# Kernel tuning notes

Measured on AMD Instinct MI355X. Metric: run time of the kernel, lower is better.

Reference implementation:

```python
import jax, jax.numpy as jnp
import numpy as np

EPS = 1e-5
KH = KW = 3
PAD = 1

def conv3x3(x, w, b=None):
    out = jax.lax.conv_general_dilated(
        x, w, window_strides=(1, 1), padding=((PAD, PAD), (PAD, PAD)),
        dimension_numbers=("NCHW", "OIHW", "NCHW"))
    if b is not None:
        out = out + b[None, :, None, None]
    return out

def batchnorm(x, gamma, beta):
    # training-mode BatchNorm2d: batch statistics over (N, H, W)
    mean = x.mean(axis=(0, 2, 3), keepdims=True)
    var = x.var(axis=(0, 2, 3), keepdims=True)
    return gamma[None, :, None, None] * (x - mean) / jnp.sqrt(var + EPS) + beta[None, :, None, None]

def bilinear_gather(x, y_pos, x_pos):
    # x: [B,C,H,W]; y_pos/x_pos: [B,P,H,W] (P = KH*KW sampling taps)
    # zero padding outside image (mmcv modulated deform conv semantics)
    B, C, H, W = x.shape
    P = y_pos.shape[1]
    x_flat = x.reshape(B, C, H * W)
    y0 = jnp.floor(y_pos)
    x0 = jnp.floor(x_pos)
    ly = y_pos - y0
    lx = x_pos - x0
    out = jnp.zeros((B, C, P, H, W), dtype=x.dtype)
    for dy, dx, wgt in ((0, 0, (1 - ly) * (1 - lx)), (0, 1, (1 - ly) * lx),
                        (1, 0, ly * (1 - lx)), (1, 1, ly * lx)):
        yi = y0 + dy
        xi = x0 + dx
        valid = ((yi >= 0) & (yi <= H - 1) & (xi >= 0) & (xi <= W - 1)).astype(x.dtype)
        yc = jnp.clip(yi, 0, H - 1).astype(jnp.int32)
        xc = jnp.clip(xi, 0, W - 1).astype(jnp.int32)
        idx = (yc * W + xc).reshape(B, 1, P * H * W)
        vals = jnp.take_along_axis(x_flat, jnp.broadcast_to(idx, (B, C, P * H * W)), axis=2)
        vals = vals.reshape(B, C, P, H, W)
        out = out + vals * (wgt * valid)[:, None]
    return out  # [B,C,P,H,W]

def modulated_deform_conv(x, w_off, b_off, w_dcn):
    B, C, H, W = x.shape
    P = KH * KW
    off = conv3x3(x, w_off, b_off)  # [B, 3*P, H, W]
    o1, o2, m = jnp.split(off, 3, axis=1)
    offset = jnp.concatenate([o1, o2], axis=1)            # [B, 2P, H, W]
    offset = offset.reshape(B, P, 2, H, W)                # channel 2p -> dy, 2p+1 -> dx
    mask = jax.nn.sigmoid(m)                              # [B, P, H, W]
    hh = jnp.arange(H, dtype=x.dtype)
    ww = jnp.arange(W, dtype=x.dtype)
    ky = jnp.arange(KH, dtype=x.dtype)
    kx = jnp.arange(KW, dtype=x.dtype)
    # base sampling grid per tap p = ky*KW + kx: (h - PAD + ky, w - PAD + kx)
    base_y = (hh[None, :] - PAD + ky[:, None])            # [KH, H]
    base_x = (ww[None, :] - PAD + kx[:, None])            # [KW, W]
    base_y = jnp.broadcast_to(base_y[:, None, :, None], (KH, KW, H, W)).reshape(P, H, W)
    base_x = jnp.broadcast_to(base_x[None, :, None, :], (KH, KW, H, W)).reshape(P, H, W)
    y_pos = base_y[None] + offset[:, :, 0]                # [B,P,H,W]
    x_pos = base_x[None] + offset[:, :, 1]
    sampled = bilinear_gather(x, y_pos, x_pos)            # [B,C,P,H,W]
    sampled = sampled * mask[:, None]
    w = w_dcn.reshape(w_dcn.shape[0], C, P)               # [O, C, P]
    return jnp.einsum("bcphw,ocp->bohw", sampled, w)

def setup_inputs() -> dict:
    key = jax.random.key(0)
    ks = jax.random.split(key, 10)
    B, Ch, H, W = 4, 256, 64, 64
    Cin, Cout = 2 * Ch, 256
    P = KH * KW
    inp = {
        "input_v": jax.random.normal(ks[0], (B, Ch, H, W), jnp.float32),
        "input_i": jax.random.normal(ks[1], (B, Ch, H, W), jnp.float32),
        "w_off": jax.random.normal(ks[2], (3 * P, Cin, KH, KW), jnp.float32) * 0.01,
        "b_off": jnp.zeros((3 * P,), jnp.float32),
        "w_dcn": jax.random.normal(ks[3], (Cout, Cin, KH, KW), jnp.float32) * (1.0 / np.sqrt(Cin * P)),
        "gamma1": jnp.ones((Cout,), jnp.float32),
        "beta1": jnp.zeros((Cout,), jnp.float32),
        "w2": jax.random.normal(ks[4], (Cout, Cout, KH, KW), jnp.float32) * (1.0 / np.sqrt(Cout * P)),
        "gamma2": jnp.ones((Cout,), jnp.float32),
        "beta2": jnp.zeros((Cout,), jnp.float32),
    }
    return inp

def reference(input_v, input_i, w_off, b_off, w_dcn, gamma1, beta1, w2, gamma2, beta2):
    x = jnp.concatenate([input_v, input_i], axis=1)
    out = modulated_deform_conv(x, w_off, b_off, w_dcn)
    out = jax.nn.relu(batchnorm(out, gamma1, beta1))
    out = jax.nn.relu(batchnorm(conv3x3(out, w2), gamma2, beta2))
    return out
```

## Files before the change

### kernel.cpp

```cpp
#include <hip/hip_runtime.h>
#include <cstdint>
#include <cstddef>

typedef unsigned short u16;
typedef __attribute__((ext_vector_type(8))) short s16x8;
typedef __attribute__((ext_vector_type(4))) float f32x4;

#define DEV __device__ __forceinline__

DEV float bf2f(short u){
  union { unsigned int i; float f; } v;
  v.i = ((unsigned int)(u16)u) << 16;
  return v.f;
}
DEV short f2bf(float f){
  union { float f; unsigned int i; } v; v.f = f;
  unsigned int u = v.i;
  u += 0x7fffu + ((u >> 16) & 1u);
  return (short)(u >> 16);
}
DEV s16x8 s16x8_zero(){
  s16x8 z;
#pragma unroll
  for(int j=0;j<8;j++) z[j]=0;
  return z;
}
DEV f32x4 f32x4_zero(){
  f32x4 z;
#pragma unroll
  for(int j=0;j<4;j++) z[j]=0.f;
  return z;
}
DEV f32x4 mfma16(s16x8 a, s16x8 b, f32x4 c){
  return __builtin_amdgcn_mfma_f32_16x16x32_bf16(a, b, c, 0, 0, 0);
}

static constexpr size_t OFF_ACC_B  = 0;
static constexpr size_t OUT1_ACC_B = 2097152;
static constexpr size_t OUT2_ACC_B = OUT1_ACC_B + 16777216;
static constexpr size_t STATS_B    = OUT2_ACC_B + 16777216;
static constexpr size_t ZERO_BYTES = STATS_B + 4096;
static constexpr size_t XN_B       = ZERO_BYTES;
static constexpr size_t OUT1N_B    = XN_B + 16777216;
static constexpr size_t WOFFT_B    = OUT1N_B + 8388608;
static constexpr size_t WDCNT_B    = WOFFT_B + 294912;
static constexpr size_t W2T_B      = WDCNT_B + 2359296;

__global__ void k_x_to_nhwc(const float* __restrict__ v, const float* __restrict__ vi,
                            u16* __restrict__ xn){
  __shared__ float tile[64][65];
  const int b = blockIdx.z, c0 = blockIdx.y*64, hw0 = blockIdx.x*64;
  const float* src = (c0 < 256) ? (v  + ((size_t)b*256 + c0)      *4096)
                                : (vi + ((size_t)b*256 + (c0-256))*4096);
  const int t = threadIdx.x;
#pragma unroll
  for(int k=0;k<16;k++){
    int idx = t + k*256;
    int cl = idx >> 6, wl = idx & 63;
    tile[cl][wl] = src[(size_t)cl*4096 + hw0 + wl];
  }
  __syncthreads();
#pragma unroll
  for(int k=0;k<16;k++){
    int idx = t + k*256;
    int wl = idx >> 6, cl = idx & 63;
    xn[(size_t)(b*4096 + hw0 + wl)*512 + c0 + cl] = (u16)f2bf(tile[cl][wl]);
  }
}

__global__ void k_prep_woff(const float* __restrict__ w, u16* __restrict__ wt){
  int idx = blockIdx.x*256 + threadIdx.x;
  if(idx >= 32*4608) return;
  int n = idx / 4608, k = idx % 4608;
  int t = k >> 9, c = k & 511;
  float val = (n < 27) ? w[(size_t)(n*512 + c)*9 + t] : 0.f;
  wt[idx] = (u16)f2bf(val);
}
__global__ void k_prep_wdcn(const float* __restrict__ w, u16* __restrict__ wt){
  int idx = blockIdx.x*256 + threadIdx.x;
  if(idx >= 256*4608) return;
  int n = idx / 4608, k = idx % 4608;
  int t = k >> 9, c = k & 511;
  wt[idx] = (u16)f2bf(w[(size_t)(n*512 + c)*9 + t]);
}
__global__ void k_prep_w2(const float* __restrict__ w, u16* __restrict__ wt){
  int idx = blockIdx.x*256 + threadIdx.x;
  if(idx >= 256*2304) return;
  int n = idx / 2304, k = idx % 2304;
  int t = k >> 8, c = k & 255;
  wt[idx] = (u16)f2bf(w[(size_t)(n*256 + c)*9 + t]);
}

__global__ __launch_bounds__(256, 2) void k_conv_off(
    const u16* __restrict__ xn, const u16* __restrict__ wt, float* __restrict__ offa){
  __shared__ short A_lds[4][128][8];
  __shared__ short B_lds[4][32][8];
  const int tid = threadIdx.x;
  const int lane = tid & 63, wid = tid >> 6;
  const int quad = lane >> 4, ln = lane & 15;
  const int m0 = blockIdx.x * 128;
  const int b = m0 >> 12;
  const int h0 = (m0 & 4095) >> 6;
  const int ks = blockIdx.y;
  const int ts0 = (ks==0)?0:(ks==1)?2:(ks==2)?4:6;
  const int ts1 = (ks==0)?2:(ks==1)?4:(ks==2)?6:9;
  const int m_base = wid * 32;
  const int r = tid >> 1, sp = (tid & 1) * 2;
  const int h_r = h0 + (r >> 6), w_r = r & 63;
  const s16x8* Ap = (const s16x8*)A_lds;
  const s16x8* Bp = (const s16x8*)B_lds;
  f32x4 acc[2][2];
#pragma unroll
  for(int mf=0;mf<2;mf++)
#pragma unroll
    for(int nf=0;nf<2;nf++) acc[mf][nf] = f32x4_zero();

  for(int tp=ts0; tp<ts1; tp++){
    const int ty = tp/3, tx = tp - ty*3;
    const int y = h_r - 1 + ty, x = w_r - 1 + tx;
    const bool vld = (y>=0) & (y<64) & (x>=0) & (x<64);
    const u16* src = xn + (long)(b*4096 + y*64 + x)*512 + sp*8;
    const int kbase = tp*512;
    for(int cc=0; cc<16; cc++){
      const int c0 = cc*32;
      s16x8 v0 = s16x8_zero(), v1 = s16x8_zero();
      if(vld){
        v0 = *(const s16x8*)(src + c0);
        v1 = *(const s16x8*)(src + c0 + 8);
      }
      *(s16x8*)(&A_lds[sp][r][0])   = v0;
      *(s16x8*)(&A_lds[sp+1][r][0]) = v1;
      if(tid < 128){
        const int n = tid & 31, s2 = tid >> 5;
        *(s16x8*)(&B_lds[s2][n][0]) =
            *(const s16x8*)(wt + (size_t)n*4608 + kbase + c0 + s2*8);
      }
      __syncthreads();
      s16x8 a0 = Ap[quad*128 + m_base + ln];
      s16x8 a1 = Ap[quad*128 + m_base + 16 + ln];
      s16x8 b0 = Bp[quad*32 + ln];
      s16x8 b1 = Bp[quad*32 + 16 + ln];
      acc[0][0] = mfma16(a0, b0, acc[0][0]);
      acc[0][1] = mfma16(a0, b1, acc[0][1]);
      acc[1][0] = mfma16(a1, b0, acc[1][0]);
      acc[1][1] = mfma16(a1, b1, acc[1][1]);
      __syncthreads();
    }
  }
#pragma unroll
  for(int mf=0;mf<2;mf++)
#pragma unroll
    for(int nf=0;nf<2;nf++){
      const int col = nf*16 + ln;
#pragma unroll
      for(int i=0;i<4;i++){
        const int row = m_base + mf*16 + quad*4 + i;
        unsafeAtomicAdd(offa + (size_t)(m0+row)*32 + col, acc[mf][nf][i]);
      }
    }
}

__global__ __launch_bounds__(256, 2) void k_dcn(
    const u16* __restrict__ xn, const u16* __restrict__ wt,
    const float* __restrict__ offa, const float* __restrict__ boff,
    float* __restrict__ outa){
  __shared__ short A_lds[4][64][8];
  __shared__ short B_lds[4][256][8];
  __shared__ int   p_ofs[4][64];
  __shared__ float p_wgt[4][64];
  const int tid = threadIdx.x;
  const int lane = tid & 63, wid = tid >> 6;
  const int quad = lane >> 4, ln = lane & 15;
  const int m0 = blockIdx.x * 64;
  const int b = m0 >> 12;
  const int h = (m0 & 4095) >> 6;
  const int ts0 = blockIdx.y ? 4 : 0;
  const int ts1 = blockIdx.y ? 9 : 4;
  const int wm = wid >> 1, wn = wid & 1;
  const int m_base = wm*32, n_base = wn*128;
  const int r = tid >> 2, sub = tid & 3;
  const s16x8* Ap = (const s16x8*)A_lds;
  const s16x8* Bp = (const s16x8*)B_lds;
  f32x4 acc[2][8];
#pragma unroll
  for(int mf=0;mf<2;mf++)
#pragma unroll
    for(int nf=0;nf<8;nf++) acc[mf][nf] = f32x4_zero();

  for(int tp=ts0; tp<ts1; tp++){
    if(tid < 64){
      const int rr = tid;
      const float* orow = offa + (size_t)(m0+rr)*32;
      float dy = orow[2*tp]   + boff[2*tp];
      float dx = orow[2*tp+1] + boff[2*tp+1];
      float mz = orow[18+tp]  + boff[18+tp];
      float mk = 1.f / (1.f + expf(-mz));
      float ypos = (float)(h - 1 + tp/3) + dy;
      float xpos = (float)(rr - 1 + tp%3) + dx;
      float y0f = floorf(ypos), x0f = floorf(xpos);
      float ly = ypos - y0f, lx = xpos - x0f;
      int y0 = (int)y0f, x0 = (int)x0f;
#pragma unroll
      for(int k=0;k<4;k++){
        int ddy = k >> 1, ddx = k & 1;
        int yi = y0 + ddy, xi = x0 + ddx;
        bool vv = (yi >= 0) & (yi < 64) & (xi >= 0) & (xi < 64);
        float wk = (ddy ? ly : 1.f-ly) * (ddx ? lx : 1.f-lx) * mk;
        if(!vv) wk = 0.f;
        int yc = yi < 0 ? 0 : (yi > 63 ? 63 : yi);
        int xc = xi < 0 ? 0 : (xi > 63 ? 63 : xi);
        p_ofs[k][rr] = ((b << 12) + (yc << 6) + xc) << 9;
        p_wgt[k][rr] = wk;
      }
    }
    __syncthreads();
    const float w0f = p_wgt[0][r], w1f = p_wgt[1][r], w2f = p_wgt[2][r], w3f = p_wgt[3][r];
    const u16* s0p = xn + p_ofs[0][r] + sub*8;
    const u16* s1p = xn + p_ofs[1][r] + sub*8;
    const u16* s2p = xn + p_ofs[2][r] + sub*8;
    const u16* s3p = xn + p_ofs[3][r] + sub*8;
    const u16* wrow0 = wt + (size_t)tid*4608 + tp*512;

    for(int cc=0; cc<16; cc++){
      const int c0 = cc*32;
      s16x8 v0 = *(const s16x8*)(s0p + c0);
      s16x8 v1 = *(const s16x8*)(s1p + c0);
      s16x8 v2 = *(const s16x8*)(s2p + c0);
      s16x8 v3 = *(const s16x8*)(s3p + c0);
      s16x8 pk;
#pragma unroll
      for(int j=0;j<8;j++){
        float f = w0f * bf2f(v0[j]);
        f = fmaf(w1f, bf2f(v1[j]), f);
        f = fmaf(w2f, bf2f(v2[j]), f);
        f = fmaf(w3f, bf2f(v3[j]), f);
        pk[j] = f2bf(f);
      }
      *(s16x8*)(&A_lds[sub][r][0]) = pk;
#pragma unroll
      for(int s2=0; s2<4; s2++)
        *(s16x8*)(&B_lds[s2][tid][0]) = *(const s16x8*)(wrow0 + c0 + s2*8);
      __syncthreads();
      s16x8 af0 = Ap[quad*64 + m_base + ln];
      s16x8 af1 = Ap[quad*64 + m_base + 16 + ln];
      s16x8 bfr[8];
#pragma unroll
      for(int nf=0;nf<8;nf++) bfr[nf] = Bp[quad*256 + n_base + nf*16 + ln];
#pragma unroll
      for(int nf=0;nf<8;nf++){
        acc[0][nf] = mfma16(af0, bfr[nf], acc[0][nf]);
        acc[1][nf] = mfma16(af1, bfr[nf], acc[1][nf]);
      }
      __syncthreads();
    }
  }
#pragma unroll
  for(int mf=0;mf<2;mf++)
#pragma unroll
    for(int nf=0;nf<8;nf++){
      const int col = n_base + nf*16 + ln;
#pragma unroll
      for(int i=0;i<4;i++){
        const int row = m_base + mf*16 + quad*4 + i;
        unsafeAtomicAdd(outa + (size_t)(m0+row)*256 + col, acc[mf][nf][i]);
      }
    }
}

__global__ __launch_bounds__(256, 2) void k_conv2(
    const u16* __restrict__ a_in, const u16* __restrict__ wt, float* __restrict__ outa){
  __shared__ short A_lds[4][64][8];
  __shared__ short B_lds[4][256][8];
  const int tid = threadIdx.x;
  const int lane = tid & 63, wid = tid >> 6;
  const int quad = lane >> 4, ln = lane & 15;
  const int m0 = blockIdx.x * 64;
  const int b = m0 >> 12;
  const int h = (m0 & 4095) >> 6;
  const int ts0 = blockIdx.y ? 4 : 0;
  const int ts1 = blockIdx.y ? 9 : 4;
  const int wm = wid >> 1, wn = wid & 1;
  const int m_base = wm*32, n_base = wn*128;
  const int r = tid >> 2, sub = tid & 3;
  const s16x8* Ap = (const s16x8*)A_lds;
  const s16x8* Bp = (const s16x8*)B_lds;
  f32x4 acc[2][8];
#pragma unroll
  for(int mf=0;mf<2;mf++)
#pragma unroll
    for(int nf=0;nf<8;nf++) acc[mf][nf] = f32x4_zero();

  for(int tp=ts0; tp<ts1; tp++){
    const int ty = tp/3, tx = tp - ty*3;
    const int y = h - 1 + ty, x = r - 1 + tx;
    const bool vld = (y>=0) & (y<64) & (x>=0) & (x<64);
    const u16* src = a_in + (long)(b*4096 + y*64 + x)*256 + sub*8;
    const u16* wrow0 = wt + (size_t)tid*2304 + tp*256;
    for(int cc=0; cc<8; cc++){
      const int c0 = cc*32;
      s16x8 va = vld ? *(const s16x8*)(src + c0) : s16x8_zero();
      *(s16x8*)(&A_lds[sub][r][0]) = va;
#pragma unroll
      for(int s2=0;s2<4;s2++)
        *(s16x8*)(&B_lds[s2][tid][0]) = *(const s16x8*)(wrow0 + c0 + s2*8);
      __syncthreads();
      s16x8 af0 = Ap[quad*64 + m_base + ln];
      s16x8 af1 = Ap[quad*64 + m_base + 16 + ln];
      s16x8 bfr[8];
#pragma unroll
      for(int nf=0;nf<8;nf++) bfr[nf] = Bp[quad*256 + n_base + nf*16 + ln];
#pragma unroll
      for(int nf=0;nf<8;nf++){
        acc[0][nf] = mfma16(af0, bfr[nf], acc[0][nf]);
        acc[1][nf] = mfma16(af1, bfr[nf], acc[1][nf]);
      }
      __syncthreads();
    }
  }
#pragma unroll
  for(int mf=0;mf<2;mf++)
#pragma unroll
    for(int nf=0;nf<8;nf++){
      const int col = n_base + nf*16 + ln;
#pragma unroll
      for(int i=0;i<4;i++){
        const int row = m_base + mf*16 + quad*4 + i;
        unsafeAtomicAdd(outa + (size_t)(m0+row)*256 + col, acc[mf][nf][i]);
      }
    }
}

__global__ void k_stats(const float* __restrict__ acc, float* __restrict__ sum,
                        float* __restrict__ sq){
  const int m0 = blockIdx.x*64;
  const int c = threadIdx.x;
  float s = 0.f, q = 0.f;
  for(int i=0;i<64;i++){
    float v = acc[(size_t)(m0+i)*256 + c];
    s += v; q += v*v;
  }
  unsafeAtomicAdd(sum + c, s);
  unsafeAtomicAdd(sq + c, q);
}

__global__ void k_bn1(const float* __restrict__ acc, const float* __restrict__ sum,
                      const float* __restrict__ sq, const float* __restrict__ g,
                      const float* __restrict__ bt, u16* __restrict__ o){
  __shared__ float sc[256], sh[256];
  const int t = threadIdx.x;
  {
    float mean = sum[t] * (1.f/16384.f);
    float var  = sq[t] * (1.f/16384.f) - mean*mean;
    float rstd = rsqrtf(var + 1e-5f);
    float s = g[t] * rstd;
    sc[t] = s; sh[t] = bt[t] - mean*s;
  }
  __syncthreads();
  const int c4 = (t & 63) * 4;
  const float s0 = sc[c4], s1 = sc[c4+1], s2 = sc[c4+2], s3 = sc[c4+3];
  const float h0 = sh[c4], h1 = sh[c4+1], h2 = sh[c4+2], h3 = sh[c4+3];
#pragma unroll
  for(int k=0;k<4;k++){
    int m = blockIdx.x*16 + k*4 + (t>>6);
    const float4 v = *(const float4*)(acc + (size_t)m*256 + c4);
    unsigned int lo = (unsigned int)(u16)f2bf(fmaxf(0.f, v.x*s0 + h0))
                    | ((unsigned int)(u16)f2bf(fmaxf(0.f, v.y*s1 + h1)) << 16);
    unsigned int hi = (unsigned int)(u16)f2bf(fmaxf(0.f, v.z*s2 + h2))
                    | ((unsigned int)(u16)f2bf(fmaxf(0.f, v.w*s3 + h3)) << 16);
    uint2 pr; pr.x = lo; pr.y = hi;
    *(uint2*)(o + (size_t)m*256 + c4) = pr;
  }
}

__global__ void k_bn2_out(const float* __restrict__ acc, const float* __restrict__ sum,
                          const float* __restrict__ sq, const float* __restrict__ g,
                          const float* __restrict__ bt, float* __restrict__ out){
  __shared__ float tile[64][65];
  __shared__ float sc[64], sh[64];
  const int t = threadIdx.x;
  const int b = blockIdx.z, c0 = blockIdx.y*64, hw0 = blockIdx.x*64;
  if(t < 64){
    int c = c0 + t;
    float mean = sum[c] * (1.f/16384.f);
    float var  = sq[c] * (1.f/16384.f) - mean*mean;
    float rstd = rsqrtf(var + 1e-5f);
    float s = g[c] * rstd;
    sc[t] = s; sh[t] = bt[c] - mean*s;
  }
  __syncthreads();
#pragma unroll
  for(int k=0;k<16;k++){
    int idx = t + k*256;
    int wl = idx >> 6, cl = idx & 63;
    float v = acc[(size_t)((b<<12) + hw0 + wl)*256 + c0 + cl];
    tile[wl][cl] = fmaxf(0.f, v*sc[cl] + sh[cl]);
  }
  __syncthreads();
#pragma unroll
  for(int k=0;k<16;k++){
    int idx = t + k*256;
    int cl = idx >> 6, wl = idx & 63;
    out[(size_t)(b*256 + c0 + cl)*4096 + hw0 + wl] = tile[wl][cl];
  }
}

extern "C" void kernel_launch(void* const* d_in, const int* in_sizes, int n_in,
                              void* d_out, int out_size, void* d_ws, size_t ws_size,
                              hipStream_t stream){
  const float* in_v  = (const float*)d_in[0];
  const float* in_i  = (const float*)d_in[1];
  const float* w_off = (const float*)d_in[2];
  const float* b_off = (const float*)d_in[3];
  const float* w_dcn = (const float*)d_in[4];
  const float* g1    = (const float*)d_in[5];
  const float* bt1   = (const float*)d_in[6];
  const float* w2    = (const float*)d_in[7];
  const float* g2    = (const float*)d_in[8];
  const float* bt2   = (const float*)d_in[9];
  float* out = (float*)d_out;
  char* ws = (char*)d_ws;

  float* off_acc  = (float*)(ws + OFF_ACC_B);
  float* out1_acc = (float*)(ws + OUT1_ACC_B);
  float* out2_acc = (float*)(ws + OUT2_ACC_B);
  float* stats    = (float*)(ws + STATS_B);
  float* sum1 = stats,       *sq1 = stats + 256;
  float* sum2 = stats + 512, *sq2 = stats + 768;
  u16* xn    = (u16*)(ws + XN_B);
  u16* out1n = (u16*)(ws + OUT1N_B);
  u16* wofft = (u16*)(ws + WOFFT_B);
  u16* wdcnt = (u16*)(ws + WDCNT_B);
  u16* w2t   = (u16*)(ws + W2T_B);

  hipMemsetAsync(ws, 0, ZERO_BYTES, stream);
  k_x_to_nhwc<<<dim3(64,8,4), 256, 0, stream>>>(in_v, in_i, xn);
  k_prep_woff<<<576, 256, 0, stream>>>(w_off, wofft);
  k_prep_wdcn<<<4608, 256, 0, stream>>>(w_dcn, wdcnt);
  k_prep_w2<<<2304, 256, 0, stream>>>(w2, w2t);
  k_conv_off<<<dim3(128,4), 256, 0, stream>>>(xn, wofft, off_acc);
  k_dcn<<<dim3(256,2), 256, 0, stream>>>(xn, wdcnt, off_acc, b_off, out1_acc);
  k_stats<<<256, 256, 0, stream>>>(out1_acc, sum1, sq1);
  k_bn1<<<1024, 256, 0, stream>>>(out1_acc, sum1, sq1, g1, bt1, out1n);
  k_conv2<<<dim3(256,2), 256, 0, stream>>>(out1n, w2t, out2_acc);
  k_stats<<<256, 256, 0, stream>>>(out2_acc, sum2, sq2);
  k_bn2_out<<<dim3(64,4,4), 256, 0, stream>>>(out2_acc, sum2, sq2, g2, bt2, out);
}
```

Measured before the change: 377.3 us.

## Software-pipeline global loads and split channels across more blocks in conv kernels

Restructures the three GEMM-style conv kernels (offset conv, deformable conv, conv2) so the next iteration's global loads are issued into registers before the LDS stores and MFMA work of the current one, hiding memory latency behind compute. Each grid doubles by splitting the input-channel range in half, and the results are combined through the existing atomic accumulation. Launch bounds go from 2 to 4 blocks per SU to raise occupancy, and the deformable kernel now computes bilinear offsets and weights for all taps up front instead of per tap. The costs are more atomic traffic, extra registers for prefetched values, and redundant per-block offset computation.

```diff
diff --git a/kernel.cpp b/kernel.cpp
--- a/kernel.cpp
+++ b/kernel.cpp
@@ -91,7 +91,7 @@
   wt[idx] = (u16)f2bf(w[(size_t)(n*256 + c)*9 + t]);
 }
 
-__global__ __launch_bounds__(256, 2) void k_conv_off(
+__global__ __launch_bounds__(256, 4) void k_conv_off(
     const u16* __restrict__ xn, const u16* __restrict__ wt, float* __restrict__ offa){
   __shared__ short A_lds[4][128][8];
   __shared__ short B_lds[4][32][8];
@@ -101,9 +101,11 @@
   const int m0 = blockIdx.x * 128;
   const int b = m0 >> 12;
   const int h0 = (m0 & 4095) >> 6;
-  const int ks = blockIdx.y;
-  const int ts0 = (ks==0)?0:(ks==1)?2:(ks==2)?4:6;
-  const int ts1 = (ks==0)?2:(ks==1)?4:(ks==2)?6:9;
+  const int ks = blockIdx.y >> 1;
+  const int chh = blockIdx.y & 1;
+  const int CH0 = chh << 8;
+  const int ts0 = (ks == 3) ? 6 : ks*2;
+  const int ntap = (ks == 3) ? 3 : 2;
   const int m_base = wid * 32;
   const int r = tid >> 1, sp = (tid & 1) * 2;
   const int h_r = h0 + (r >> 6), w_r = r & 63;
@@ -115,37 +117,45 @@
 #pragma unroll
     for(int nf=0;nf<2;nf++) acc[mf][nf] = f32x4_zero();
 
-  for(int tp=ts0; tp<ts1; tp++){
+  s16x8 v0, v1, bv;
+  auto load_it = [&](int it){
+    const int tp = ts0 + (it >> 3);
     const int ty = tp/3, tx = tp - ty*3;
     const int y = h_r - 1 + ty, x = w_r - 1 + tx;
     const bool vld = (y>=0) & (y<64) & (x>=0) & (x<64);
-    const u16* src = xn + (long)(b*4096 + y*64 + x)*512 + sp*8;
-    const int kbase = tp*512;
-    for(int cc=0; cc<16; cc++){
-      const int c0 = cc*32;
-      s16x8 v0 = s16x8_zero(), v1 = s16x8_zero();
-      if(vld){
-        v0 = *(const s16x8*)(src + c0);
-        v1 = *(const s16x8*)(src + c0 + 8);
-      }
-      *(s16x8*)(&A_lds[sp][r][0])   = v0;
-      *(s16x8*)(&A_lds[sp+1][r][0]) = v1;
-      if(tid < 128){
-        const int n = tid & 31, s2 = tid >> 5;
-        *(s16x8*)(&B_lds[s2][n][0]) =
-            *(const s16x8*)(wt + (size_t)n*4608 + kbase + c0 + s2*8);
-      }
-      __syncthreads();
-      s16x8 a0 = Ap[quad*128 + m_base + ln];
-      s16x8 a1 = Ap[quad*128 + m_base + 16 + ln];
-      s16x8 b0 = Bp[quad*32 + ln];
-      s16x8 b1 = Bp[quad*32 + 16 + ln];
-      acc[0][0] = mfma16(a0, b0, acc[0][0]);
-      acc[0][1] = mfma16(a0, b1, acc[0][1]);
-      acc[1][0] = mfma16(a1, b0, acc[1][0]);
-      acc[1][1] = mfma16(a1, b1, acc[1][1]);
-      __syncthreads();
-    }
+    const int cA = CH0 + (it & 7)*32;
+    v0 = s16x8_zero(); v1 = s16x8_zero();
+    if(vld){
+      const u16* src = xn + ((size_t)((b<<12) + (y<<6) + x) << 9) + cA + sp*8;
+      v0 = *(const s16x8*)(src);
+      v1 = *(const s16x8*)(src + 8);
+    }
+    if(tid < 128){
+      const int n = tid & 31, s2 = tid >> 5;
+      bv = *(const s16x8*)(wt + (size_t)n*4608 + tp*512 + cA + s2*8);
+    }
+  };
+
+  const int NIT = ntap * 8;
+  load_it(0);
+  for(int it = 0; it < NIT; ++it){
+    __syncthreads();
+    *(s16x8*)(&A_lds[sp][r][0])   = v0;
+    *(s16x8*)(&A_lds[sp+1][r][0]) = v1;
+    if(tid < 128){
+      const int n = tid & 31, s2 = tid >> 5;
+      *(s16x8*)(&B_lds[s2][n][0]) = bv;
+    }
+    if(it + 1 < NIT) load_it(it + 1);
+    __syncthreads();
+    s16x8 a0 = Ap[quad*128 + m_base + ln];
+    s16x8 a1 = Ap[quad*128 + m_base + 16 + ln];
+    s16x8 b0 = Bp[quad*32 + ln];
+    s16x8 b1 = Bp[quad*32 + 16 + ln];
+    acc[0][0] = mfma16(a0, b0, acc[0][0]);
+    acc[0][1] = mfma16(a0, b1, acc[0][1]);
+    acc[1][0] = mfma16(a1, b0, acc[1][0]);
+    acc[1][1] = mfma16(a1, b1, acc[1][1]);
   }
 #pragma unroll
   for(int mf=0;mf<2;mf++)
@@ -160,37 +170,42 @@
     }
 }
 
-__global__ __launch_bounds__(256, 2) void k_dcn(
+__global__ __launch_bounds__(256, 4) void k_dcn(
     const u16* __restrict__ xn, const u16* __restrict__ wt,
     const float* __restrict__ offa, const float* __restrict__ boff,
     float* __restrict__ outa){
   __shared__ short A_lds[4][64][8];
   __shared__ short B_lds[4][256][8];
-  __shared__ int   p_ofs[4][64];
-  __shared__ float p_wgt[4][64];
+  __shared__ int   p_ofs[5][4][64];
+  __shared__ float p_wgt[5][4][64];
   const int tid = threadIdx.x;
   const int lane = tid & 63, wid = tid >> 6;
   const int quad = lane >> 4, ln = lane & 15;
   const int m0 = blockIdx.x * 64;
   const int b = m0 >> 12;
   const int h = (m0 & 4095) >> 6;
-  const int ts0 = blockIdx.y ? 4 : 0;
-  const int ts1 = blockIdx.y ? 9 : 4;
+  const int tg = blockIdx.y >> 1;
+  const int chh = blockIdx.y & 1;
+  const int CH0 = chh << 8;
+  const int ts0 = tg ? 4 : 0;
+  const int ntap = tg ? 5 : 4;
   const int wm = wid >> 1, wn = wid & 1;
   const int m_base = wm*32, n_base = wn*128;
   const int r = tid >> 2, sub = tid & 3;
   const s16x8* Ap = (const s16x8*)A_lds;
   const s16x8* Bp = (const s16x8*)B_lds;
+  const u16* wrowt = wt + (size_t)tid*4608;
   f32x4 acc[2][8];
 #pragma unroll
   for(int mf=0;mf<2;mf++)
 #pragma unroll
     for(int nf=0;nf<8;nf++) acc[mf][nf] = f32x4_zero();
 
-  for(int tp=ts0; tp<ts1; tp++){
-    if(tid < 64){
-      const int rr = tid;
-      const float* orow = offa + (size_t)(m0+rr)*32;
+  {
+    const int rr = tid & 63;
+    const float* orow = offa + (size_t)(m0+rr)*32;
+    for(int tpi = tid >> 6; tpi < ntap; tpi += 4){
+      const int tp = ts0 + tpi;
       float dy = orow[2*tp]   + boff[2*tp];
       float dx = orow[2*tp+1] + boff[2*tp+1];
       float mz = orow[18+tp]  + boff[18+tp];
@@ -209,49 +224,64 @@
         if(!vv) wk = 0.f;
         int yc = yi < 0 ? 0 : (yi > 63 ? 63 : yi);
         int xc = xi < 0 ? 0 : (xi > 63 ? 63 : xi);
-        p_ofs[k][rr] = ((b << 12) + (yc << 6) + xc) << 9;
-        p_wgt[k][rr] = wk;
+        p_ofs[tpi][k][rr] = ((b << 12) + (yc << 6) + xc) << 9;
+        p_wgt[tpi][k][rr] = wk;
       }
     }
-    __syncthreads();
-    const float w0f = p_wgt[0][r], w1f = p_wgt[1][r], w2f = p_wgt[2][r], w3f = p_wgt[3][r];
-    const u16* s0p = xn + p_ofs[0][r] + sub*8;
-    const u16* s1p = xn + p_ofs[1][r] + sub*8;
-    const u16* s2p = xn + p_ofs[2][r] + sub*8;
-    const u16* s3p = xn + p_ofs[3][r] + sub*8;
-    const u16* wrow0 = wt + (size_t)tid*4608 + tp*512;
-
-    for(int cc=0; cc<16; cc++){
-      const int c0 = cc*32;
-      s16x8 v0 = *(const s16x8*)(s0p + c0);
-      s16x8 v1 = *(const s16x8*)(s1p + c0);
-      s16x8 v2 = *(const s16x8*)(s2p + c0);
-      s16x8 v3 = *(const s16x8*)(s3p + c0);
-      s16x8 pk;
-#pragma unroll
-      for(int j=0;j<8;j++){
-        float f = w0f * bf2f(v0[j]);
-        f = fmaf(w1f, bf2f(v1[j]), f);
-        f = fmaf(w2f, bf2f(v2[j]), f);
-        f = fmaf(w3f, bf2f(v3[j]), f);
-        pk[j] = f2bf(f);
-      }
-      *(s16x8*)(&A_lds[sub][r][0]) = pk;
-#pragma unroll
-      for(int s2=0; s2<4; s2++)
-        *(s16x8*)(&B_lds[s2][tid][0]) = *(const s16x8*)(wrow0 + c0 + s2*8);
-      __syncthreads();
-      s16x8 af0 = Ap[quad*64 + m_base + ln];
-      s16x8 af1 = Ap[quad*64 + m_base + 16 + ln];
-      s16x8 bfr[8];
-#pragma unroll
-      for(int nf=0;nf<8;nf++) bfr[nf] = Bp[quad*256 + n_base + nf*16 + ln];
-#pragma unroll
-      for(int nf=0;nf<8;nf++){
-        acc[0][nf] = mfma16(af0, bfr[nf], acc[0][nf]);
-        acc[1][nf] = mfma16(af1, bfr[nf], acc[1][nf]);
-      }
-      __syncthreads();
+  }
+  __syncthreads();
+
+  s16x8 a0, a1, a2, a3, b0, b1, b2, b3;
+  float w0, w1, w2, w3;
+  auto loadA = [&](int it){
+    const int tpi = it >> 3;
+    const int c0 = CH0 + (it & 7)*32 + sub*8;
+    w0 = p_wgt[tpi][0][r]; w1 = p_wgt[tpi][1][r];
+    w2 = p_wgt[tpi][2][r]; w3 = p_wgt[tpi][3][r];
+    a0 = *(const s16x8*)(xn + p_ofs[tpi][0][r] + c0);
+    a1 = *(const s16x8*)(xn + p_ofs[tpi][1][r] + c0);
+    a2 = *(const s16x8*)(xn + p_ofs[tpi][2][r] + c0);
+    a3 = *(const s16x8*)(xn + p_ofs[tpi][3][r] + c0);
+  };
+  auto loadB = [&](int it){
+    const int kb = (ts0 + (it >> 3))*512 + CH0 + (it & 7)*32;
+    b0 = *(const s16x8*)(wrowt + kb);
+    b1 = *(const s16x8*)(wrowt + kb + 8);
+    b2 = *(const s16x8*)(wrowt + kb + 16);
+    b3 = *(const s16x8*)(wrowt + kb + 24);
+  };
+
+  const int NIT = ntap * 8;
+  loadA(0); loadB(0);
+  for(int it = 0; it < NIT; ++it){
+    s16x8 pk;
+#pragma unroll
+    for(int j=0;j<8;j++){
+      float f = w0 * bf2f(a0[j]);
+      f = fmaf(w1, bf2f(a1[j]), f);
+      f = fmaf(w2, bf2f(a2[j]), f);
+      f = fmaf(w3, bf2f(a3[j]), f);
+      pk[j] = f2bf(f);
+    }
+    const bool more = (it + 1 < NIT);
+    if(more) loadA(it + 1);
+    __syncthreads();
+    *(s16x8*)(&A_lds[sub][r][0]) = pk;
+    *(s16x8*)(&B_lds[0][tid][0]) = b0;
+    *(s16x8*)(&B_lds[1][tid][0]) = b1;
+    *(s16x8*)(&B_lds[2][tid][0]) = b2;
+    *(s16x8*)(&B_lds[3][tid][0]) = b3;
+    if(more) loadB(it + 1);
+    __syncthreads();
+    s16x8 af0 = Ap[quad*64 + m_base + ln];
+    s16x8 af1 = Ap[quad*64 + m_base + 16 + ln];
+    s16x8 bfr[8];
+#pragma unroll
+    for(int nf=0;nf<8;nf++) bfr[nf] = Bp[quad*256 + n_base + nf*16 + ln];
+#pragma unroll
+    for(int nf=0;nf<8;nf++){
+      acc[0][nf] = mfma16(af0, bfr[nf], acc[0][nf]);
+      acc[1][nf] = mfma16(af1, bfr[nf], acc[1][nf]);
     }
   }
 #pragma unroll
@@ -267,7 +297,7 @@
     }
 }
 
-__global__ __launch_bounds__(256, 2) void k_conv2(
+__global__ __launch_bounds__(256, 4) void k_conv2(
     const u16* __restrict__ a_in, const u16* __restrict__ wt, float* __restrict__ outa){
   __shared__ short A_lds[4][64][8];
   __shared__ short B_lds[4][256][8];
@@ -277,44 +307,59 @@
   const int m0 = blockIdx.x * 64;
   const int b = m0 >> 12;
   const int h = (m0 & 4095) >> 6;
-  const int ts0 = blockIdx.y ? 4 : 0;
-  const int ts1 = blockIdx.y ? 9 : 4;
+  const int tg = blockIdx.y >> 1;
+  const int chh = blockIdx.y & 1;
+  const int CH0 = chh << 7;
+  const int ts0 = tg ? 4 : 0;
+  const int ntap = tg ? 5 : 4;
   const int wm = wid >> 1, wn = wid & 1;
   const int m_base = wm*32, n_base = wn*128;
   const int r = tid >> 2, sub = tid & 3;
   const s16x8* Ap = (const s16x8*)A_lds;
   const s16x8* Bp = (const s16x8*)B_lds;
+  const u16* wrowt = wt + (size_t)tid*2304;
   f32x4 acc[2][8];
 #pragma unroll
   for(int mf=0;mf<2;mf++)
 #pragma unroll
     for(int nf=0;nf<8;nf++) acc[mf][nf] = f32x4_zero();
 
-  for(int tp=ts0; tp<ts1; tp++){
+  s16x8 va, b0, b1, b2, b3;
+  auto load_it = [&](int it){
+    const int tp = ts0 + (it >> 2);
     const int ty = tp/3, tx = tp - ty*3;
     const int y = h - 1 + ty, x = r - 1 + tx;
     const bool vld = (y>=0) & (y<64) & (x>=0) & (x<64);
-    const u16* src = a_in + (long)(b*4096 + y*64 + x)*256 + sub*8;
-    const u16* wrow0 = wt + (size_t)tid*2304 + tp*256;
-    for(int cc=0; cc<8; cc++){
-      const int c0 = cc*32;
-      s16x8 va = vld ? *(const s16x8*)(src + c0) : s16x8_zero();
-      *(s16x8*)(&A_lds[sub][r][0]) = va;
-#pragma unroll
-      for(int s2=0;s2<4;s2++)
-        *(s16x8*)(&B_lds[s2][tid][0]) = *(const s16x8*)(wrow0 + c0 + s2*8);
-      __syncthreads();
-      s16x8 af0 = Ap[quad*64 + m_base + ln];
-      s16x8 af1 = Ap[quad*64 + m_base + 16 + ln];
-      s16x8 bfr[8];
-#pragma unroll
-      for(int nf=0;nf<8;nf++) bfr[nf] = Bp[quad*256 + n_base + nf*16 + ln];
-#pragma unroll
-      for(int nf=0;nf<8;nf++){
-        acc[0][nf] = mfma16(af0, bfr[nf], acc[0][nf]);
-        acc[1][nf] = mfma16(af1, bfr[nf], acc[1][nf]);
-      }
-      __syncthreads();
+    const int c0 = CH0 + (it & 3)*32;
+    va = s16x8_zero();
+    if(vld) va = *(const s16x8*)(a_in + (((size_t)((b<<12) + (y<<6) + x)) << 8) + c0 + sub*8);
+    const int kb = tp*256 + c0;
+    b0 = *(const s16x8*)(wrowt + kb);
+    b1 = *(const s16x8*)(wrowt + kb + 8);
+    b2 = *(const s16x8*)(wrowt + kb + 16);
+    b3 = *(const s16x8*)(wrowt + kb + 24);
+  };
+
+  const int NIT = ntap * 4;
+  load_it(0);
+  for(int it = 0; it < NIT; ++it){
+    __syncthreads();
+    *(s16x8*)(&A_lds[sub][r][0]) = va;
+    *(s16x8*)(&B_lds[0][tid][0]) = b0;
+    *(s16x8*)(&B_lds[1][tid][0]) = b1;
+    *(s16x8*)(&B_lds[2][tid][0]) = b2;
+    *(s16x8*)(&B_lds[3][tid][0]) = b3;
+    if(it + 1 < NIT) load_it(it + 1);
+    __syncthreads();
+    s16x8 af0 = Ap[quad*64 + m_base + ln];
+    s16x8 af1 = Ap[quad*64 + m_base + 16 + ln];
+    s16x8 bfr[8];
+#pragma unroll
+    for(int nf=0;nf<8;nf++) bfr[nf] = Bp[quad*256 + n_base + nf*16 + ln];
+#pragma unroll
+    for(int nf=0;nf<8;nf++){
+      acc[0][nf] = mfma16(af0, bfr[nf], acc[0][nf]);
+      acc[1][nf] = mfma16(af1, bfr[nf], acc[1][nf]);
     }
   }
 #pragma unroll
@@ -437,11 +482,11 @@
   k_prep_woff<<<576, 256, 0, stream>>>(w_off, wofft);
   k_prep_wdcn<<<4608, 256, 0, stream>>>(w_dcn, wdcnt);
   k_prep_w2<<<2304, 256, 0, stream>>>(w2, w2t);
-  k_conv_off<<<dim3(128,4), 256, 0, stream>>>(xn, wofft, off_acc);
-  k_dcn<<<dim3(256,2), 256, 0, stream>>>(xn, wdcnt, off_acc, b_off, out1_acc);
+  k_conv_off<<<dim3(128,8), 256, 0, stream>>>(xn, wofft, off_acc);
+  k_dcn<<<dim3(256,4), 256, 0, stream>>>(xn, wdcnt, off_acc, b_off, out1_acc);
   k_stats<<<256, 256, 0, stream>>>(out1_acc, sum1, sq1);
   k_bn1<<<1024, 256, 0, stream>>>(out1_acc, sum1, sq1, g1, bt1, out1n);
-  k_conv2<<<dim3(256,2), 256, 0, stream>>>(out1n, w2t, out2_acc);
+  k_conv2<<<dim3(256,4), 256, 0, stream>>>(out1n, w2t, out2_acc);
   k_stats<<<256, 256, 0, stream>>>(out2_acc, sum2, sq2);
   k_bn2_out<<<dim3(64,4,4), 256, 0, stream>>>(out2_acc, sum2, sq2, g2, bt2, out);
 }
```

Measured after the change: 396.9 us. 1.05x slower.
